# Kernel tuning notes

Measured on AMD Instinct MI355X. Metric: run time of the kernel, lower is better.

Reference implementation:

```python
import jax, jax.numpy as jnp
import numpy as np

B, T, E, H = 8, 2048, 1024, 128

def setup_inputs() -> dict:
    key = jax.random.key(0)
    k1, k2, k3, k4 = jax.random.split(key, 4)
    s = 0.02
    return {
        "x":  jax.random.normal(k1, (B, T, E), dtype=jnp.float32),
        "Wq": jax.random.normal(k2, (E, H), dtype=jnp.float32) * s,
        "Wk": jax.random.normal(k3, (E, H), dtype=jnp.float32) * s,
        "Wv": jax.random.normal(k4, (E, H), dtype=jnp.float32) * s,
    }

def reference(x, Wq, Wk, Wv):
    # q,k,v: [B,T,H]
    q = jnp.einsum("bte,eh->bth", x, Wq)
    k = jnp.einsum("bte,eh->bth", x, Wk)
    v = jnp.einsum("bte,eh->bth", x, Wv)
    scale = jnp.asarray(q.shape[-1], q.dtype) ** -0.5
    wei = jnp.einsum("bqh,bkh->bqk", q, k) * scale  # [B,T,T]
    causal = jnp.tril(jnp.ones((wei.shape[1], wei.shape[2]), dtype=bool))
    wei = jnp.where(causal, wei, jnp.asarray(-jnp.inf, wei.dtype))
    wei = jax.nn.softmax(wei, axis=-1)
    # dropout_prob = 0.0 -> identity
    return jnp.einsum("bqk,bkh->bqh", wei, v)
```

## Files before the change

### kernel.cpp

```cpp
#include <hip/hip_runtime.h>

#define BB 8
#define TT 2048
#define EE 1024
#define HH 128

typedef __bf16 bf16;
typedef __attribute__((ext_vector_type(8))) __bf16 bf16x8;
typedef __attribute__((ext_vector_type(4))) __bf16 bf16x4;
typedef __attribute__((ext_vector_type(4))) float f32x4;
typedef __attribute__((ext_vector_type(16))) float f32x16;

__device__ __host__ inline int qb_off(int qb) {
  int h = qb >> 1;
  return qb + h * (h - 1) + ((qb & 1) ? h : 0);
}
#define NSLAB 72

__device__ inline void gload_lds16(const bf16* g, bf16* l) {
  __builtin_amdgcn_global_load_lds((const __attribute__((address_space(1))) unsigned int*)g,
                                   (__attribute__((address_space(3))) unsigned int*)l,
                                   16, 0, 0);
}

__global__ __launch_bounds__(256) void wt_kernel(const float* __restrict__ wq,
                                                 const float* __restrict__ wk,
                                                 const float* __restrict__ wv,
                                                 bf16* __restrict__ wt) {
  __shared__ float tile[64][65];
  const int z = blockIdx.z;
  const float* w = (z == 0) ? wq : ((z == 1) ? wk : wv);
  const int k0 = blockIdx.x * 64;
  const int h0 = blockIdx.y * 64;
  const int c = threadIdx.x & 63;
  const int r0 = threadIdx.x >> 6;
#pragma unroll
  for (int i = 0; i < 16; ++i) {
    int tt = r0 + i * 4;
    tile[tt][c] = w[(size_t)(k0 + tt) * HH + h0 + c];
  }
  __syncthreads();
#pragma unroll
  for (int i = 0; i < 16; ++i) {
    int hh = r0 + i * 4;
    wt[((size_t)(z * HH + h0 + hh)) * EE + k0 + c] = (bf16)tile[c][hh];
  }
}

__global__ __launch_bounds__(256) void gemm_kernel(const float* __restrict__ x,
                                                   const bf16* __restrict__ wt,
                                                   bf16* __restrict__ q,
                                                   bf16* __restrict__ k,
                                                   bf16* __restrict__ vt) {
  __shared__ bf16 As[2][128 * 32];
  __shared__ bf16 Bs[2][96 * 32];
  const int tid = threadIdx.x;
  const int lane = tid & 63;
  const int wave = tid >> 6;
  const int l16 = lane & 15;
  const int quad = lane >> 4;
  const int wm = wave & 1;
  const int wn = wave >> 1;
  const int bm = blockIdx.x;
  const int ntile = blockIdx.y;

  const int trow = tid >> 2;
  const int tsub = (tid & 3) * 8;
  const float* gA = x + (size_t)(bm * 128 + trow) * EE + tsub;
  const bf16* gB = wt + (size_t)(ntile * 96 + trow) * EE + tsub;
  const int awr = trow * 32 + tsub;

  f32x4 acc[4][3];
#pragma unroll
  for (int rg = 0; rg < 4; ++rg)
#pragma unroll
    for (int nt = 0; nt < 3; ++nt) acc[rg][nt] = f32x4{0.f, 0.f, 0.f, 0.f};

  auto stageB = [&](int bufi, int ks) {
    gload_lds16(gB + ks * 32, &Bs[bufi][wave * 512]);
    if (tid < 128)
      gload_lds16(gB + (size_t)64 * EE + ks * 32, &Bs[bufi][2048 + wave * 512]);
  };
  auto packA = [](f32x4 a0, f32x4 a1) {
    bf16x8 ab;
#pragma unroll
    for (int jj = 0; jj < 4; ++jj) { ab[jj] = (bf16)a0[jj]; ab[jj + 4] = (bf16)a1[jj]; }
    return ab;
  };

  {
    f32x4 a0 = *(const f32x4*)(gA);
    f32x4 a1 = *(const f32x4*)(gA + 4);
    f32x4 a2 = *(const f32x4*)(gA + (size_t)64 * EE);
    f32x4 a3 = *(const f32x4*)(gA + (size_t)64 * EE + 4);
    stageB(0, 0);
    *(bf16x8*)&As[0][awr] = packA(a0, a1);
    *(bf16x8*)&As[0][2048 + awr] = packA(a2, a3);
  }
  __syncthreads();

  int buf = 0;
  for (int ks = 0; ks < EE / 32; ++ks) {
    bf16x8 af[4], bf_[3];
#pragma unroll
    for (int rg = 0; rg < 4; ++rg)
      af[rg] = *(const bf16x8*)&As[buf][(wm * 64 + rg * 16 + l16) * 32 + quad * 8];
#pragma unroll
    for (int nt = 0; nt < 3; ++nt)
      bf_[nt] = *(const bf16x8*)&Bs[buf][(wn * 48 + nt * 16 + l16) * 32 + quad * 8];

    f32x4 a0, a1, a2, a3;
    if (ks < EE / 32 - 1) {
      const float* gn = gA + (ks + 1) * 32;
      a0 = *(const f32x4*)(gn);
      a1 = *(const f32x4*)(gn + 4);
      a2 = *(const f32x4*)(gn + (size_t)64 * EE);
      a3 = *(const f32x4*)(gn + (size_t)64 * EE + 4);
      stageB(buf ^ 1, ks + 1);
    }

#pragma unroll
    for (int rg = 0; rg < 4; ++rg)
#pragma unroll
      for (int nt = 0; nt < 3; ++nt)
        acc[rg][nt] = __builtin_amdgcn_mfma_f32_16x16x32_bf16(af[rg], bf_[nt], acc[rg][nt], 0, 0, 0);

    if (ks < EE / 32 - 1) {
      *(bf16x8*)&As[buf ^ 1][awr] = packA(a0, a1);
      *(bf16x8*)&As[buf ^ 1][2048 + awr] = packA(a2, a3);
    }
    __syncthreads();
    buf ^= 1;
  }

#pragma unroll
  for (int rg = 0; rg < 4; ++rg)
#pragma unroll
    for (int nt = 0; nt < 3; ++nt) {
      int col = ntile * 96 + wn * 48 + nt * 16 + l16;
      int z = col >> 7;
      int n = col & 127;
      int row0 = bm * 128 + wm * 64 + rg * 16 + quad * 4;
      if (z == 2) {
        int bb = row0 >> 11;
        int t0 = row0 & (TT - 1);
        bf16x4 pkv;
#pragma unroll
        for (int r = 0; r < 4; ++r) pkv[r] = (bf16)acc[rg][nt][r];
        *(bf16x4*)&vt[((size_t)(bb * HH + n)) * TT + t0] = pkv;
      } else {
        bf16* op = (z == 0) ? q : k;
#pragma unroll
        for (int r = 0; r < 4; ++r)
          op[(size_t)(row0 + r) * HH + n] = (bf16)acc[rg][nt][r];
      }
    }
}

__device__ __forceinline__ unsigned pk2(float a, float b) {
  union { __bf16 h[2]; unsigned u; } x;
  x.h[0] = (__bf16)a;
  x.h[1] = (__bf16)b;
  return x.u;
}

__device__ __forceinline__ void plswap(unsigned& a, unsigned& b) {
  asm volatile("v_permlane32_swap_b32 %0, %1" : "+v"(a), "+v"(b));
}

__global__ __launch_bounds__(256, 2) void flash_kernel(const bf16* __restrict__ q,
                                                       const bf16* __restrict__ k,
                                                       const bf16* __restrict__ vt,
                                                       bf16* __restrict__ opart,
                                                       float* __restrict__ lpart) {
  __shared__ bf16 Ks[2][64 * 128];
  __shared__ bf16 Vs[128 * 64];

  const int b = blockIdx.x & 7;
  int j = (NSLAB - 1) - (blockIdx.x >> 3);
  int qb = 0, ns = 1;
  while (j >= ns) { j -= ns; ++qb; ns = ((2 * qb + 1) >> 2) + 1; }
  const int s = j;
  const int kt0 = s * 4;
  const int kt1 = min(kt0 + 3, 2 * qb + 1);

  const int tid = threadIdx.x;
  const int lane = tid & 63;
  const int wave = tid >> 6;
  const int l32 = lane & 31;
  const int hi = lane >> 5;
  const int qrow = qb * 128 + wave * 32 + l32;
  const int kdiag = qb * 4 + wave;

  bf16x8 qf[8];
  {
    const bf16* qp = q + (size_t)(b * TT + qrow) * HH + hi * 8;
#pragma unroll
    for (int h16 = 0; h16 < 8; ++h16) qf[h16] = *(const bf16x8*)(qp + h16 * 16);
  }

  f32x16 O[4];
#pragma unroll
  for (int ht = 0; ht < 4; ++ht)
#pragma unroll
    for (int r = 0; r < 16; ++r) O[ht][r] = 0.f;
  float L = 0.f;

  const int krow_s = tid >> 4;
  const int kchk_s = (tid & 15) ^ (krow_s & 7);
  const int vrow_s = tid >> 3;
  const int vchk_s = (tid & 7) ^ (vrow_s & 7);
  const bf16* kg = k + (size_t)b * TT * HH;
  const bf16* vg = vt + (size_t)b * HH * TT;

  auto stageK = [&](int bufi, int kt) {
#pragma unroll
    for (int i = 0; i < 4; ++i)
      gload_lds16(kg + (size_t)(kt * 64 + i * 16 + krow_s) * HH + kchk_s * 8,
                  &Ks[bufi][(i * 256 + wave * 64) * 8]);
  };
  auto stageV = [&](int kt) {
#pragma unroll
    for (int i = 0; i < 4; ++i)
      gload_lds16(vg + (size_t)(i * 32 + vrow_s) * TT + kt * 64 + vchk_s * 8,
                  &Vs[(i * 256 + wave * 64) * 8]);
  };

  const int kxor = (l32 & 7) << 3;
  const float c_ = 0.12753257680406733f;

  stageK(0, kt0);
  stageV(kt0);
  __syncthreads();

  int buf = 0;
  for (int kt = kt0; kt <= kt1; ++kt) {
    if (kt < kt1) stageK(buf ^ 1, kt + 1);

#pragma unroll
    for (int khalf = 0; khalf < 2; ++khalf) {
      const int k32 = kt * 2 + khalf;
      if (k32 <= kdiag) {
        const bf16* kls = &Ks[buf][(khalf * 32 + l32) * 128];
        bf16x8 kf[8];
#pragma unroll
        for (int h16 = 0; h16 < 8; ++h16)
          kf[h16] = *(const bf16x8*)&kls[(h16 * 16 + hi * 8) ^ kxor];

        f32x16 S;
#pragma unroll
        for (int r = 0; r < 16; ++r) S[r] = 0.f;
        __builtin_amdgcn_s_setprio(1);
#pragma unroll
        for (int h16 = 0; h16 < 8; ++h16)
          S = __builtin_amdgcn_mfma_f32_32x32x16_bf16(kf[h16], qf[h16], S, 0, 0, 0);
        __builtin_amdgcn_s_setprio(0);

        float p[16];
        if (k32 == kdiag) {
          const int kkb = k32 * 32 + 4 * hi;
#pragma unroll
          for (int r = 0; r < 16; ++r) {
            int kk = kkb + (r & 3) + 8 * (r >> 2);
            p[r] = (kk <= qrow) ? exp2f(S[r] * c_) : 0.f;
          }
        } else {
#pragma unroll
          for (int r = 0; r < 16; ++r) p[r] = exp2f(S[r] * c_);
        }
        L += (((p[0] + p[1]) + (p[2] + p[3])) + ((p[4] + p[5]) + (p[6] + p[7]))) +
             (((p[8] + p[9]) + (p[10] + p[11])) + ((p[12] + p[13]) + (p[14] + p[15])));

#pragma unroll
        for (int s16 = 0; s16 < 2; ++s16) {
          unsigned w0 = pk2(p[s16 * 8 + 0], p[s16 * 8 + 1]);
          unsigned w1 = pk2(p[s16 * 8 + 2], p[s16 * 8 + 3]);
          unsigned w2 = pk2(p[s16 * 8 + 4], p[s16 * 8 + 5]);
          unsigned w3 = pk2(p[s16 * 8 + 6], p[s16 * 8 + 7]);
          plswap(w0, w2);
          plswap(w1, w3);
          union { unsigned u[4]; bf16x8 v; } af;
          af.u[0] = w0;
          af.u[1] = w1;
          af.u[2] = w2;
          af.u[3] = w3;
          bf16x8 vf[4];
#pragma unroll
          for (int ht = 0; ht < 4; ++ht)
            vf[ht] = *(const bf16x8*)&Vs[(l32 + 32 * ht) * 64 +
                                         ((khalf * 32 + s16 * 16 + hi * 8) ^ kxor)];
          __builtin_amdgcn_s_setprio(1);
#pragma unroll
          for (int ht = 0; ht < 4; ++ht)
            O[ht] = __builtin_amdgcn_mfma_f32_32x32x16_bf16(af.v, vf[ht], O[ht], 0, 0, 0);
          __builtin_amdgcn_s_setprio(0);
        }
      }
    }
    __syncthreads();
    if (kt < kt1) {
      stageV(kt + 1);
      __syncthreads();
    }
    buf ^= 1;
  }

  L += __shfl_xor(L, 32, 64);

  const size_t slab = (size_t)(b * NSLAB + qb_off(qb) + s);
  bf16* op = opart + slab * (128 * 128) + (size_t)wave * 32 * 128;
#pragma unroll
  for (int ht = 0; ht < 4; ++ht)
#pragma unroll
    for (int r = 0; r < 16; ++r) {
      int qr = (r & 3) + 8 * (r >> 2) + 4 * hi;
      op[qr * 128 + ht * 32 + l32] = (bf16)O[ht][r];
    }
  if (hi == 0) lpart[slab * 128 + wave * 32 + l32] = L;
}

__global__ __launch_bounds__(128) void combine_kernel(const bf16* __restrict__ opart,
                                                      const float* __restrict__ lpart,
                                                      float* __restrict__ out) {
  const int b = blockIdx.x;
  const int qt16 = blockIdx.y;
  const int half = blockIdx.z;
  const int row = threadIdx.x >> 3;
  const int colo = (threadIdx.x & 7) * 8 + half * 64;
  const int qb = qt16 >> 3;
  const int srow = (qt16 & 7) * 16 + row;
  const int ns = ((2 * qb + 1) >> 2) + 1;
  const size_t slab0 = (size_t)(b * NSLAB + qb_off(qb));

  float acc[8];
#pragma unroll
  for (int j = 0; j < 8; ++j) acc[j] = 0.f;
  float L = 0.f;

  int s = 0;
  for (; s + 4 <= ns; s += 4) {
    float l0 = lpart[(slab0 + s + 0) * 128 + srow];
    float l1 = lpart[(slab0 + s + 1) * 128 + srow];
    float l2 = lpart[(slab0 + s + 2) * 128 + srow];
    float l3 = lpart[(slab0 + s + 3) * 128 + srow];
    bf16x8 v0 = *(const bf16x8*)(opart + (slab0 + s + 0) * (128 * 128) + srow * 128 + colo);
    bf16x8 v1 = *(const bf16x8*)(opart + (slab0 + s + 1) * (128 * 128) + srow * 128 + colo);
    bf16x8 v2 = *(const bf16x8*)(opart + (slab0 + s + 2) * (128 * 128) + srow * 128 + colo);
    bf16x8 v3 = *(const bf16x8*)(opart + (slab0 + s + 3) * (128 * 128) + srow * 128 + colo);
    L += (l0 + l1) + (l2 + l3);
#pragma unroll
    for (int j = 0; j < 8; ++j)
      acc[j] += ((float)v0[j] + (float)v1[j]) + ((float)v2[j] + (float)v3[j]);
  }
  for (; s < ns; ++s) {
    L += lpart[(slab0 + s) * 128 + srow];
    bf16x8 ov = *(const bf16x8*)(opart + (slab0 + s) * (128 * 128) + srow * 128 + colo);
#pragma unroll
    for (int j = 0; j < 8; ++j) acc[j] += (float)ov[j];
  }
  float invL = 1.f / L;
  float* o = out + ((size_t)(b * TT + qt16 * 16 + row)) * HH + colo;
  f32x4 o0, o1;
#pragma unroll
  for (int j = 0; j < 4; ++j) { o0[j] = acc[j] * invL; o1[j] = acc[j + 4] * invL; }
  *(f32x4*)o = o0;
  *(f32x4*)(o + 4) = o1;
}

extern "C" void kernel_launch(void* const* d_in, const int* in_sizes, int n_in,
                              void* d_out, int out_size, void* d_ws, size_t ws_size,
                              hipStream_t stream) {
  const float* x = (const float*)d_in[0];
  const float* wq = (const float*)d_in[1];
  const float* wk = (const float*)d_in[2];
  const float* wv = (const float*)d_in[3];
  float* out = (float*)d_out;

  char* ws = (char*)d_ws;
  const size_t NE = (size_t)BB * TT * HH;
  bf16* wt = (bf16*)ws;
  bf16* q = (bf16*)(ws + (1 << 20));
  bf16* k = q + NE;
  bf16* vt = k + NE;
  bf16* opart = (bf16*)(ws + (16 << 20));
  float* lpart = (float*)(opart + (size_t)(BB * NSLAB) * 128 * 128);

  wt_kernel<<<dim3(16, 2, 3), 256, 0, stream>>>(wq, wk, wv, wt);
  gemm_kernel<<<dim3(128, 4), 256, 0, stream>>>(x, wt, q, k, vt);
  flash_kernel<<<dim3(576), 256, 0, stream>>>(q, k, vt, opart, lpart);
  combine_kernel<<<dim3(8, 128, 2), 128, 0, stream>>>(opart, lpart, out);
}
```

Baseline: 160.4 us.

## Pad A tile in LDS and prefetch x two K-steps ahead in QKV GEMM

The A (x) tile in shared memory gets a padded row stride of 40 instead of 32, so MFMA fragment reads hit fewer LDS bank conflicts. Global loads of x are now issued two K-steps ahead into alternating register sets, with the K loop unrolled by two to ping-pong them. This hides more global-load latency behind MFMA work, at the cost of extra registers and slightly more LDS.

```diff
diff --git a/kernel.cpp b/kernel.cpp
--- a/kernel.cpp
+++ b/kernel.cpp
@@ -52,7 +52,7 @@
                                                    bf16* __restrict__ q,
                                                    bf16* __restrict__ k,
                                                    bf16* __restrict__ vt) {
-  __shared__ bf16 As[2][128 * 32];
+  __shared__ bf16 As[2][128 * 40];
   __shared__ bf16 Bs[2][96 * 32];
   const int tid = threadIdx.x;
   const int lane = tid & 63;
@@ -68,7 +68,7 @@
   const int tsub = (tid & 3) * 8;
   const float* gA = x + (size_t)(bm * 128 + trow) * EE + tsub;
   const bf16* gB = wt + (size_t)(ntile * 96 + trow) * EE + tsub;
-  const int awr = trow * 32 + tsub;
+  const int awr = trow * 40 + tsub;
 
   f32x4 acc[4][3];
 #pragma unroll
@@ -81,43 +81,44 @@
     if (tid < 128)
       gload_lds16(gB + (size_t)64 * EE + ks * 32, &Bs[bufi][2048 + wave * 512]);
   };
-  auto packA = [](f32x4 a0, f32x4 a1) {
-    bf16x8 ab;
-#pragma unroll
-    for (int jj = 0; jj < 4; ++jj) { ab[jj] = (bf16)a0[jj]; ab[jj + 4] = (bf16)a1[jj]; }
-    return ab;
-  };
-
+  auto loadA = [&](int ks, f32x4* r) {
+    const float* gn = gA + ks * 32;
+    r[0] = *(const f32x4*)(gn);
+    r[1] = *(const f32x4*)(gn + 4);
+    r[2] = *(const f32x4*)(gn + (size_t)64 * EE);
+    r[3] = *(const f32x4*)(gn + (size_t)64 * EE + 4);
+  };
+  auto writeA = [&](int bufi, const f32x4* r) {
+    bf16x8 ab0, ab1;
+#pragma unroll
+    for (int jj = 0; jj < 4; ++jj) {
+      ab0[jj] = (bf16)r[0][jj]; ab0[jj + 4] = (bf16)r[1][jj];
+      ab1[jj] = (bf16)r[2][jj]; ab1[jj + 4] = (bf16)r[3][jj];
+    }
+    *(bf16x8*)&As[bufi][awr] = ab0;
+    *(bf16x8*)&As[bufi][64 * 40 + awr] = ab1;
+  };
+
+  f32x4 rA0[4], rA1[4];
   {
-    f32x4 a0 = *(const f32x4*)(gA);
-    f32x4 a1 = *(const f32x4*)(gA + 4);
-    f32x4 a2 = *(const f32x4*)(gA + (size_t)64 * EE);
-    f32x4 a3 = *(const f32x4*)(gA + (size_t)64 * EE + 4);
+    loadA(0, rA0);
     stageB(0, 0);
-    *(bf16x8*)&As[0][awr] = packA(a0, a1);
-    *(bf16x8*)&As[0][2048 + awr] = packA(a2, a3);
+    writeA(0, rA0);
+    loadA(1, rA1);
   }
   __syncthreads();
 
-  int buf = 0;
-  for (int ks = 0; ks < EE / 32; ++ks) {
+  auto body = [&](int ks, int buf, f32x4* rIssue, f32x4* rWrite) {
     bf16x8 af[4], bf_[3];
 #pragma unroll
     for (int rg = 0; rg < 4; ++rg)
-      af[rg] = *(const bf16x8*)&As[buf][(wm * 64 + rg * 16 + l16) * 32 + quad * 8];
+      af[rg] = *(const bf16x8*)&As[buf][(wm * 64 + rg * 16 + l16) * 40 + quad * 8];
 #pragma unroll
     for (int nt = 0; nt < 3; ++nt)
       bf_[nt] = *(const bf16x8*)&Bs[buf][(wn * 48 + nt * 16 + l16) * 32 + quad * 8];
 
-    f32x4 a0, a1, a2, a3;
-    if (ks < EE / 32 - 1) {
-      const float* gn = gA + (ks + 1) * 32;
-      a0 = *(const f32x4*)(gn);
-      a1 = *(const f32x4*)(gn + 4);
-      a2 = *(const f32x4*)(gn + (size_t)64 * EE);
-      a3 = *(const f32x4*)(gn + (size_t)64 * EE + 4);
-      stageB(buf ^ 1, ks + 1);
-    }
+    if (ks + 2 < EE / 32) loadA(ks + 2, rIssue);
+    if (ks + 1 < EE / 32) stageB(buf ^ 1, ks + 1);
 
 #pragma unroll
     for (int rg = 0; rg < 4; ++rg)
@@ -125,12 +126,13 @@
       for (int nt = 0; nt < 3; ++nt)
         acc[rg][nt] = __builtin_amdgcn_mfma_f32_16x16x32_bf16(af[rg], bf_[nt], acc[rg][nt], 0, 0, 0);
 
-    if (ks < EE / 32 - 1) {
-      *(bf16x8*)&As[buf ^ 1][awr] = packA(a0, a1);
-      *(bf16x8*)&As[buf ^ 1][2048 + awr] = packA(a2, a3);
-    }
+    if (ks + 1 < EE / 32) writeA(buf ^ 1, rWrite);
     __syncthreads();
-    buf ^= 1;
+  };
+
+  for (int ks = 0; ks < EE / 32; ks += 2) {
+    body(ks, 0, rA0, rA1);
+    body(ks + 1, 1, rA1, rA0);
   }
 
 #pragma unroll
```

Result: faster. 157.1 us (-2.1%).
